# Kernel tuning notes

Measured on AMD Instinct MI355X. Metric: run time of the kernel, lower is better.

The kernel has to match this reference:

```python
import jax, jax.numpy as jnp
import numpy as np

D_MODEL = 1024
NUM_HEADS = 16
HEAD_DIM = D_MODEL // NUM_HEADS
THETA = 10000.0
BATCH, SEQ = 2, 2048


def rope(x, token_positions):
    # x: [b, h, s, d]; token_positions: [s]
    d = x.shape[-1]
    freqs = 1.0 / THETA ** (jnp.arange(0, d, 2, dtype=jnp.float32)[: d // 2] / d)
    ang = token_positions.astype(jnp.float32)[:, None] * freqs[None, :]  # [s, d/2]
    cos, sin = jnp.cos(ang), jnp.sin(ang)
    xr = x.reshape(*x.shape[:-1], d // 2, 2)
    x_even, x_odd = xr[..., 0], xr[..., 1]
    out_even = x_even * cos - x_odd * sin
    out_odd = x_even * sin + x_odd * cos
    return jnp.stack([out_even, out_odd], axis=-1).reshape(x.shape)


def setup_inputs() -> dict:
    key = jax.random.key(0)
    ks = jax.random.split(key, 5)
    std = np.sqrt(2.0 / (D_MODEL + D_MODEL))
    mk = lambda k: (jax.random.truncated_normal(k, -3.0, 3.0, (D_MODEL, D_MODEL), jnp.float32) * std)
    return {
        "x": jax.random.normal(ks[0], (BATCH, SEQ, D_MODEL), jnp.float32),
        "Wq": mk(ks[1]),
        "Wk": mk(ks[2]),
        "Wv": mk(ks[3]),
        "Wo": mk(ks[4]),
        "casual_mask": jnp.tril(jnp.ones((SEQ, SEQ), dtype=bool)),
        "token_positions": jnp.arange(SEQ, dtype=jnp.int32),
    }


def reference(x, Wq, Wk, Wv, Wo, casual_mask, token_positions):
    b, s, _ = x.shape
    split = lambda t: t.reshape(b, s, NUM_HEADS, HEAD_DIM).transpose(0, 2, 1, 3)
    q = split(x @ Wq.T)  # [b, h, s, d]
    k = split(x @ Wk.T)
    v = split(x @ Wv.T)
    q = rope(q, token_positions)
    k = rope(k, token_positions)
    scores = jnp.einsum("bhqd,bhkd->bhqk", q, k) / np.sqrt(HEAD_DIM)
    scores = jnp.where(casual_mask, scores, -jnp.inf)
    probs = jax.nn.softmax(scores, axis=-1)
    out = jnp.einsum("bhqk,bhkd->bhqd", probs, v)
    out = out.transpose(0, 2, 1, 3).reshape(b, s, D_MODEL)
    return out @ Wo.T
```

## Files before the change

### kernel.cpp

```cpp
#include <hip/hip_runtime.h>
#include <hip/hip_bf16.h>

#define SEQ_LEN 2048
#define NBATCH 2
#define DM 1024
#define NH 16
#define HD 64
#define NR (NBATCH * SEQ_LEN)
#define NQKV (3 * DM)
#define LDQK 2048

typedef __attribute__((ext_vector_type(8))) short bf16x8;
typedef __attribute__((ext_vector_type(4))) float f32x4;
typedef __attribute__((ext_vector_type(16))) float f32x16;

__device__ __forceinline__ short f2b(float f) {
    __hip_bfloat16 h = __float2bfloat16(f);
    return *reinterpret_cast<short*>(&h);
}

__device__ __forceinline__ void gload_lds16(const void* g, void* l) {
    __builtin_amdgcn_global_load_lds(
        (const __attribute__((address_space(1))) unsigned int*)g,
        (__attribute__((address_space(3))) unsigned int*)l, 16, 0, 0);
}

__global__ __launch_bounds__(256) void cvt_all(
    const float* __restrict__ x,  const float* __restrict__ wq,
    const float* __restrict__ wk, const float* __restrict__ wv,
    const float* __restrict__ wo,
    __hip_bfloat16* __restrict__ xb, __hip_bfloat16* __restrict__ wqkvb,
    __hip_bfloat16* __restrict__ wob) {
    int id = blockIdx.x;
    const float* src; __hip_bfloat16* dst;
    if (id < 4096) { src = x + (size_t)id * 1024; dst = xb + (size_t)id * 1024; }
    else {
        int k = id - 4096, seg = k >> 10;
        size_t off = (size_t)(k & 1023) * 1024;
        if      (seg == 0) { src = wq + off; dst = wqkvb + off; }
        else if (seg == 1) { src = wk + off; dst = wqkvb + (1u << 20) + off; }
        else if (seg == 2) { src = wv + off; dst = wqkvb + (2u << 20) + off; }
        else               { src = wo + off; dst = wob + off; }
    }
    int i = threadIdx.x * 4;
    float4 v = *(const float4*)(src + i);
    dst[i + 0] = __float2bfloat16(v.x);
    dst[i + 1] = __float2bfloat16(v.y);
    dst[i + 2] = __float2bfloat16(v.z);
    dst[i + 3] = __float2bfloat16(v.w);
}

__device__ __forceinline__ void store_c(float* p, float v) { *p = v; }
__device__ __forceinline__ void store_c(__hip_bfloat16* p, float v) {
    *p = __float2bfloat16(v);
}

template <typename CT, bool FUSED>
__global__ __launch_bounds__(256) void gemm128(
    const __hip_bfloat16* __restrict__ A,
    const __hip_bfloat16* __restrict__ B,
    CT* __restrict__ C, int K, int ldc,
    __hip_bfloat16* __restrict__ Vtg, const int* __restrict__ pos, int nbx) {
    __shared__ __hip_bfloat16 As[2][128 * 32];
    __shared__ __hip_bfloat16 Bs[2][128 * 32];
    const int t    = threadIdx.x;
    const int wave = t >> 6;
    const int lane = t & 63;
    const int quad = lane >> 4;
    const int l16  = lane & 15;
    const int wy = wave >> 1, wx = wave & 1;

    const int nwg = gridDim.x;
    const int wg  = (blockIdx.x & 7) * (nwg >> 3) + (blockIdx.x >> 3);
    const int bx  = wg % nbx;
    const int by  = wg / nbx;
    const int m0 = bx * 128, n0 = by * 128;

    const int sr  = t >> 2;
    const int scx = (t & 3) ^ (sr & 3);

    const __hip_bfloat16* Ag = A + (size_t)(m0 + sr) * K + scx * 8;
    const __hip_bfloat16* Bg = B + (size_t)(n0 + sr) * K + scx * 8;

#define GSTAGE(BUF, K0)                                                         \
    {                                                                           \
        gload_lds16(Ag + (K0), (char*)As[BUF] + t * 16);                        \
        gload_lds16(Ag + (size_t)64 * K + (K0), (char*)As[BUF] + (t + 256) * 16); \
        gload_lds16(Bg + (K0), (char*)Bs[BUF] + t * 16);                        \
        gload_lds16(Bg + (size_t)64 * K + (K0), (char*)Bs[BUF] + (t + 256) * 16); \
    }

    f32x4 acc[4][4];
#pragma unroll
    for (int i = 0; i < 4; i++)
#pragma unroll
        for (int j = 0; j < 4; j++) acc[i][j] = (f32x4){0.f, 0.f, 0.f, 0.f};

    const int NT = K >> 5;
    GSTAGE(0, 0);
    __syncthreads();
    int cur = 0;
    for (int t32 = 0; t32 < NT; ++t32) {
        if (t32 + 1 < NT) GSTAGE(cur ^ 1, (t32 + 1) * 32);

        bf16x8 af[4], bfr[4];
#pragma unroll
        for (int rb = 0; rb < 4; rb++) {
            int row = wy * 64 + rb * 16 + l16;
            af[rb] = *(const bf16x8*)((const char*)As[cur] + row * 64 +
                                      ((quad ^ (row & 3)) << 4));
        }
#pragma unroll
        for (int cb = 0; cb < 4; cb++) {
            int row = wx * 64 + cb * 16 + l16;
            bfr[cb] = *(const bf16x8*)((const char*)Bs[cur] + row * 64 +
                                       ((quad ^ (row & 3)) << 4));
        }
#pragma unroll
        for (int rb = 0; rb < 4; rb++)
#pragma unroll
            for (int cb = 0; cb < 4; cb++)
                acc[rb][cb] = __builtin_amdgcn_mfma_f32_16x16x32_bf16(
                    af[rb], bfr[cb], acc[rb][cb], 0, 0, 0);

        __syncthreads();
        cur ^= 1;
    }
#undef GSTAGE

    if (!FUSED || by < 16) {
        if constexpr (FUSED) {
            const float sc = (by < 8) ? 0.125f : 1.0f;
            float fr[4];
#pragma unroll
            for (int cb = 0; cb < 4; cb++) {
                int i = ((cb * 16 + l16) & 63) >> 1;
                fr[cb] = __expf(-(float)(2 * i) * (9.210340371976184f / 64.0f));
            }
            const float par = (l16 & 1) ? 1.f : -1.f;
#pragma unroll
            for (int rb = 0; rb < 4; rb++)
#pragma unroll
                for (int r = 0; r < 4; r++) {
                    int row = m0 + wy * 64 + rb * 16 + quad * 4 + r;
                    float p = (float)pos[row & (SEQ_LEN - 1)];
#pragma unroll
                    for (int cb = 0; cb < 4; cb++) {
                        float sn, cs;
                        __sincosf(p * fr[cb], &sn, &cs);
                        float v  = acc[rb][cb][r];
                        float pt = __shfl_xor(v, 1);
                        acc[rb][cb][r] = (v * cs + par * pt * sn) * sc;
                    }
                }
        }
#pragma unroll
        for (int rb = 0; rb < 4; rb++)
#pragma unroll
            for (int r = 0; r < 4; r++) {
                size_t ro = (size_t)(m0 + wy * 64 + rb * 16 + quad * 4 + r) * ldc;
#pragma unroll
                for (int cb = 0; cb < 4; cb++)
                    store_c(&C[ro + n0 + wx * 64 + cb * 16 + l16], acc[rb][cb][r]);
            }
    } else {
#pragma unroll
        for (int rb = 0; rb < 4; rb++) {
            int row0 = m0 + wy * 64 + rb * 16 + quad * 4;
            int bb = row0 >> 11, ss = row0 & (SEQ_LEN - 1);
            int ssw = (ss & ~12) | ((ss & 4) << 1) | ((ss & 8) >> 1);
#pragma unroll
            for (int cb = 0; cb < 4; cb++) {
                int vcol = n0 + wx * 64 + cb * 16 + l16 - 2048;
                int hh = vcol >> 6, dd = vcol & 63;
                ushort4 u;
                u.x = (unsigned short)f2b(acc[rb][cb][0]);
                u.y = (unsigned short)f2b(acc[rb][cb][1]);
                u.z = (unsigned short)f2b(acc[rb][cb][2]);
                u.w = (unsigned short)f2b(acc[rb][cb][3]);
                *(ushort4*)(Vtg + ((size_t)(bb * NH + hh) * HD + dd) * SEQ_LEN + ssw) = u;
            }
        }
    }
}

__global__ __launch_bounds__(256, 2) void attn_kernel(
    const __hip_bfloat16* __restrict__ QK,
    const __hip_bfloat16* __restrict__ Vtg,
    __hip_bfloat16* __restrict__ O) {
    __shared__ __hip_bfloat16 Ks[2][64 * 64];
    __shared__ __hip_bfloat16 Vs[2][64 * 64];

    const int t    = threadIdx.x;
    const int wave = t >> 6;
    const int lane = t & 63;
    const int l5   = lane & 31;
    const int hi   = lane >> 5;
    const int id   = blockIdx.x;
    const int qtc  = id >> 5;
    const int hb   = id & 31;
    const int h    = hb & 15;
    const int b    = hb >> 4;
    const int qt   = (qtc < 8) ? (15 - qtc) : (qtc - 8);

    const int row0 = qt * 128 + wave * 32;
    const int ktd  = (row0 + 31) >> 6;
    const int KTM  = 2 * qt + 1;

    const int sr  = t >> 3;
    const int scx = (t & 7) ^ (sr & 7);

    const __hip_bfloat16* kbase = QK + (size_t)(b * SEQ_LEN) * LDQK + DM + h * HD;
    const __hip_bfloat16* vbase = Vtg + (size_t)((b * NH + h) * HD) * SEQ_LEN;

    bf16x8 qf[4];
    {
        const __hip_bfloat16* qp =
            QK + (size_t)(b * SEQ_LEN + row0 + l5) * LDQK + h * HD + hi * 8;
#pragma unroll
        for (int dc = 0; dc < 4; dc++) qf[dc] = *(const bf16x8*)(qp + dc * 16);
    }

    f32x16 o0, o1;
#pragma unroll
    for (int i = 0; i < 16; i++) { o0[i] = 0.f; o1[i] = 0.f; }
    float l_acc = 0.f;

#define STAGE(BUF, KT)                                                          \
    {                                                                           \
        gload_lds16(kbase + (size_t)((KT) * 64 + sr) * LDQK + scx * 8,          \
                    (char*)&Ks[BUF][0] + t * 16);                               \
        gload_lds16(kbase + (size_t)((KT) * 64 + sr + 32) * LDQK + scx * 8,     \
                    (char*)&Ks[BUF][0] + (t + 256) * 16);                       \
        gload_lds16(vbase + (size_t)sr * SEQ_LEN + (KT) * 64 + scx * 8,         \
                    (char*)&Vs[BUF][0] + t * 16);                               \
        gload_lds16(vbase + (size_t)(sr + 32) * SEQ_LEN + (KT) * 64 + scx * 8,  \
                    (char*)&Vs[BUF][0] + (t + 256) * 16);                       \
    }

#define LFRAG(BASE, ROW, CH)                                                    \
    (*(const bf16x8*)((const char*)(BASE) + (ROW) * 128 + ((((CH) ^ ((ROW) & 7))) << 4)))

#define MKPA(S, PA0, PA1)                                                       \
    {                                                                           \
        float p_[16];                                                           \
        _Pragma("unroll") for (int r = 0; r < 16; r++) {                        \
            p_[r] = __expf((S)[r]);                                             \
            l_acc += p_[r];                                                     \
        }                                                                       \
        _Pragma("unroll") for (int j = 0; j < 8; j++) {                         \
            PA0[j] = f2b(p_[j]);                                                \
            PA1[j] = f2b(p_[8 + j]);                                            \
        }                                                                       \
    }

#define TRIP(BUF, KT)                                                           \
    {                                                                           \
        f32x16 s0, s1;                                                          \
        _Pragma("unroll") for (int i = 0; i < 16; i++) { s0[i] = 0.f; s1[i] = 0.f; } \
        __builtin_amdgcn_s_setprio(1);                                          \
        _Pragma("unroll") for (int dc = 0; dc < 4; dc++) {                      \
            bf16x8 k0f = LFRAG(Ks[BUF], l5, dc * 2 + hi);                       \
            bf16x8 k1f = LFRAG(Ks[BUF], 32 + l5, dc * 2 + hi);                  \
            s0 = __builtin_amdgcn_mfma_f32_32x32x16_bf16(k0f, qf[dc], s0, 0, 0, 0); \
            s1 = __builtin_amdgcn_mfma_f32_32x32x16_bf16(k1f, qf[dc], s1, 0, 0, 0); \
        }                                                                       \
        __builtin_amdgcn_s_setprio(0);                                          \
        if ((KT) == ktd) {                \
            int qrow = row0 + l5;                                               \
            _Pragma("unroll") for (int r = 0; r < 16; r++) {                    \
                int key = (KT) * 64 + (r & 3) + 8 * (r >> 2) + 4 * hi;          \
                if (key > qrow) s0[r] = -1e30f;                                 \
                if (key + 32 > qrow) s1[r] = -1e30f;                            \
            }                                                                   \
        }                                                                       \
        bf16x8 pa0, pa1, pa2, pa3;                                              \
        MKPA(s0, pa0, pa1);                                                     \
        MKPA(s1, pa2, pa3);                                                     \
        __builtin_amdgcn_s_setprio(1);                                          \
        _Pragma("unroll") for (int kc = 0; kc < 4; kc++) {                      \
            bf16x8 v0f = LFRAG(Vs[BUF], l5, kc * 2 + hi);                       \
            bf16x8 v1f = LFRAG(Vs[BUF], 32 + l5, kc * 2 + hi);                  \
            bf16x8 paf = (kc == 0) ? pa0 : (kc == 1) ? pa1 : (kc == 2) ? pa2 : pa3; \
            o0 = __builtin_amdgcn_mfma_f32_32x32x16_bf16(paf, v0f, o0, 0, 0, 0); \
            o1 = __builtin_amdgcn_mfma_f32_32x32x16_bf16(paf, v1f, o1, 0, 0, 0); \
        }                                                                       \
        __builtin_amdgcn_s_setprio(0);                                          \
    }

    STAGE(0, 0);
    for (int kt = 0; kt <= KTM; ++kt) {
        const int buf = kt & 1;
        __syncthreads();
        if (kt < KTM) STAGE(buf ^ 1, kt + 1);
        if (kt <= ktd) TRIP(buf, kt);
    }

    l_acc += __shfl_xor(l_acc, 32);
    float inv = 1.0f / l_acc;
#pragma unroll
    for (int r = 0; r < 16; r++) {
        int crow  = (r & 3) + 8 * (r >> 2) + 4 * hi;
        float invr = __shfl(inv, crow);
        size_t ro = (size_t)(b * SEQ_LEN + row0 + crow) * DM + h * HD;
        O[ro + l5]      = __float2bfloat16(o0[r] * invr);
        O[ro + 32 + l5] = __float2bfloat16(o1[r] * invr);
    }
#undef STAGE
#undef LFRAG
#undef MKPA
#undef TRIP
}

extern "C" void kernel_launch(void* const* d_in, const int* in_sizes, int n_in,
                              void* d_out, int out_size, void* d_ws, size_t ws_size,
                              hipStream_t stream) {
    const float* x  = (const float*)d_in[0];
    const float* Wq = (const float*)d_in[1];
    const float* Wk = (const float*)d_in[2];
    const float* Wv = (const float*)d_in[3];
    const float* Wo = (const float*)d_in[4];
    const int* pos = (const int*)d_in[6];
    float* out = (float*)d_out;

    char* w = (char*)d_ws;
    const size_t MiB = 1024 * 1024;
    __hip_bfloat16* xb    = (__hip_bfloat16*)(w + 0 * MiB);
    __hip_bfloat16* Ab    = (__hip_bfloat16*)(w + 0 * MiB);
    __hip_bfloat16* Wqkvb = (__hip_bfloat16*)(w + 8 * MiB);
    __hip_bfloat16* Wob   = (__hip_bfloat16*)(w + 14 * MiB);
    __hip_bfloat16* QKb   = (__hip_bfloat16*)(w + 16 * MiB);
    __hip_bfloat16* Vtg   = (__hip_bfloat16*)(w + 32 * MiB);

    cvt_all<<<8192, 256, 0, stream>>>(x, Wq, Wk, Wv, Wo, xb, Wqkvb, Wob);

    gemm128<__hip_bfloat16, true><<<(NR / 128) * (NQKV / 128), 256, 0, stream>>>(
        xb, Wqkvb, QKb, DM, LDQK, Vtg, pos, NR / 128);

    attn_kernel<<<512, 256, 0, stream>>>(QKb, Vtg, Ab);

    gemm128<float, false><<<(NR / 128) * (DM / 128), 256, 0, stream>>>(
        Ab, Wob, out, DM, DM, nullptr, nullptr, NR / 128);
}
```

Before: 196.5 us.

## Replace QKV projection GEMM with 256x256-tile, 8-wave pipelined kernel

Adds a dedicated QKV projection kernel that uses 256x256 output tiles with 512 threads, split into quarter-tile LDS stages that are double-buffered. Global loads are interleaved with the MFMA sub-blocks and controlled by explicit vmcnt waits and barriers. The RoPE, scaling and V-transpose epilogue are reimplemented inline. The larger tiles increase data reuse and cut global traffic per FLOP. In exchange the grid drops to 192 workgroups, which may underfill the 256 CUs, and register pressure goes up.

```diff
diff --git a/kernel.cpp b/kernel.cpp
--- a/kernel.cpp
+++ b/kernel.cpp
@@ -55,6 +55,197 @@
     *p = __float2bfloat16(v);
 }
 
+__global__ __launch_bounds__(512) void gemm256_qkv(
+    const __hip_bfloat16* __restrict__ A,
+    const __hip_bfloat16* __restrict__ B,
+    __hip_bfloat16* __restrict__ C,
+    __hip_bfloat16* __restrict__ Vtg,
+    const int* __restrict__ pos) {
+    __shared__ __hip_bfloat16 As[2][2][64 * 128];
+    __shared__ __hip_bfloat16 Bs[2][2][64 * 128];
+
+    const int t    = threadIdx.x;
+    const int wave = t >> 6;
+    const int wm   = wave >> 2;
+    const int wn   = wave & 3;
+    const int lane = t & 63;
+    const int quad = lane >> 4;
+    const int l16  = lane & 15;
+    const int K    = DM;
+    const int NT   = K >> 6;
+    const int NI   = K >> 7;
+
+    const int wg = (blockIdx.x & 7) * 24 + (blockIdx.x >> 3);
+    const int bx = wg & 15;
+    const int by = wg >> 4;
+    const int m0 = bx * 256, n0 = by * 256;
+
+    const int  t16  = t * 16;
+    const int  scx8 = ((t & 7) ^ ((t >> 3) & 7)) * 8;
+    const int  srA  = t >> 3;
+    const int  gB   = (t >> 8) & 1;
+    const int  rB   = (t >> 3) & 31;
+
+#define STAGE_A(BUF, HM, TT)                                                    \
+    {                                                                           \
+        const __hip_bfloat16* _s =                                              \
+            A + (size_t)(m0 + (HM) * 64 + srA) * K + (TT) * 64 + scx8;          \
+        gload_lds16(_s,               (char*)As[BUF][HM] + t16);                \
+        gload_lds16(_s + (size_t)128 * K, (char*)As[BUF][HM] + t16 + 8192);     \
+    }
+#define STAGE_B(BUF, HN, TT)                                                    \
+    {                                                                           \
+        const __hip_bfloat16* _s =                                              \
+            B + (size_t)(n0 + gB * 64 + (HN) * 32 + rB) * K + (TT) * 64 + scx8; \
+        gload_lds16(_s,               (char*)Bs[BUF][HN] + t16);                \
+        gload_lds16(_s + (size_t)128 * K, (char*)Bs[BUF][HN] + t16 + 8192);     \
+    }
+#define LDA(BUF, HM, AF)                                                        \
+    _Pragma("unroll") for (int rb = 0; rb < 4; rb++)                            \
+    _Pragma("unroll") for (int kk = 0; kk < 2; kk++)                            \
+        AF[rb][kk] = *(const bf16x8*)((const char*)As[BUF][HM] +                \
+            (wm * 64 + rb * 16 + l16) * 128 + (((kk * 4 + quad) ^ (l16 & 7)) << 4));
+#define LDB(BUF, HN, BF)                                                        \
+    _Pragma("unroll") for (int cb = 0; cb < 2; cb++)                            \
+    _Pragma("unroll") for (int kk = 0; kk < 2; kk++)                            \
+        BF[cb][kk] = *(const bf16x8*)((const char*)Bs[BUF][HN] +                \
+            (wn * 32 + cb * 16 + l16) * 128 + (((kk * 4 + quad) ^ (l16 & 7)) << 4));
+#define MM(HM, HN, AF, BF)                                                      \
+    {                                                                           \
+        __builtin_amdgcn_s_setprio(1);                                          \
+        _Pragma("unroll") for (int rb = 0; rb < 4; rb++)                        \
+        _Pragma("unroll") for (int cb = 0; cb < 2; cb++) {                      \
+            acc[HM][HN][rb][cb] = __builtin_amdgcn_mfma_f32_16x16x32_bf16(      \
+                AF[rb][0], BF[cb][0], acc[HM][HN][rb][cb], 0, 0, 0);            \
+            acc[HM][HN][rb][cb] = __builtin_amdgcn_mfma_f32_16x16x32_bf16(      \
+                AF[rb][1], BF[cb][1], acc[HM][HN][rb][cb], 0, 0, 0);            \
+        }                                                                       \
+        __builtin_amdgcn_s_setprio(0);                                          \
+    }
+#define VM0 asm volatile("s_waitcnt vmcnt(0)" ::: "memory")
+#define VM4 asm volatile("s_waitcnt vmcnt(4)" ::: "memory")
+#define VM6 asm volatile("s_waitcnt vmcnt(6)" ::: "memory")
+#define BARR __builtin_amdgcn_s_barrier()
+
+    f32x4 acc[2][2][4][2];
+#pragma unroll
+    for (int a_ = 0; a_ < 2; a_++)
+#pragma unroll
+        for (int b_ = 0; b_ < 2; b_++)
+#pragma unroll
+            for (int c_ = 0; c_ < 4; c_++)
+#pragma unroll
+                for (int d_ = 0; d_ < 2; d_++)
+                    acc[a_][b_][c_][d_] = (f32x4){0.f, 0.f, 0.f, 0.f};
+
+    STAGE_A(0, 0, 0); STAGE_A(0, 1, 0); STAGE_B(0, 0, 0); STAGE_B(0, 1, 0);
+    STAGE_A(1, 0, 1); STAGE_B(1, 0, 1); STAGE_A(1, 1, 1);
+    VM6;
+    BARR;
+
+    for (int i = 0; i < NI; ++i) {
+        const int TB = 2 * i + 1, T2 = 2 * i + 2, T3 = 2 * i + 3;
+        const bool s2 = T2 < NT, s3 = T3 < NT;
+        bf16x8 a[4][2], b0[2][2], b1[2][2];
+
+        LDA(0, 0, a); LDB(0, 0, b0);
+        STAGE_B(1, 1, TB);
+        MM(0, 0, a, b0);
+        BARR;
+        LDB(0, 1, b1);
+        if (s2) STAGE_A(0, 0, T2);
+        MM(0, 1, a, b1);
+        BARR;
+        LDA(0, 1, a); LDB(0, 0, b0);
+        MM(1, 0, a, b0);
+        BARR;
+        LDB(0, 1, b1);
+        if (s2) STAGE_B(0, 0, T2);
+        MM(1, 1, a, b1);
+        if (i < NI - 1) { VM4; } else { VM0; }
+        BARR;
+        LDA(1, 0, a); LDB(1, 0, b0);
+        if (s2) STAGE_A(0, 1, T2);
+        MM(0, 0, a, b0);
+        BARR;
+        LDB(1, 1, b1);
+        if (s2) STAGE_B(0, 1, T2);
+        if (s3) STAGE_A(1, 0, T3);
+        MM(0, 1, a, b1);
+        BARR;
+        LDA(1, 1, a); LDB(1, 0, b0);
+        MM(1, 0, a, b0);
+        BARR;
+        LDB(1, 1, b1);
+        if (s3) { STAGE_B(1, 0, T3); STAGE_A(1, 1, T3); }
+        MM(1, 1, a, b1);
+        if (i < NI - 1) { VM6; BARR; }
+    }
+#undef STAGE_A
+#undef STAGE_B
+#undef LDA
+#undef LDB
+#undef MM
+#undef VM0
+#undef VM4
+#undef VM6
+#undef BARR
+
+    if (by < 8) {
+        const float sc = (by < 4) ? 0.125f : 1.0f;
+        float fr[2][2];
+#pragma unroll
+        for (int hn = 0; hn < 2; hn++)
+#pragma unroll
+            for (int cb = 0; cb < 2; cb++)
+                fr[hn][cb] = __expf(-(float)((hn * 32 + cb * 16 + l16) & ~1) *
+                                    (9.210340371976184f / 64.0f));
+        const float par = (l16 & 1) ? 1.f : -1.f;
+#pragma unroll
+        for (int hm = 0; hm < 2; hm++)
+#pragma unroll
+            for (int rb = 0; rb < 4; rb++)
+#pragma unroll
+                for (int r = 0; r < 4; r++) {
+                    int row = m0 + wm * 128 + hm * 64 + rb * 16 + quad * 4 + r;
+                    float p = (float)pos[row & (SEQ_LEN - 1)];
+#pragma unroll
+                    for (int hn = 0; hn < 2; hn++)
+#pragma unroll
+                        for (int cb = 0; cb < 2; cb++) {
+                            float sn, cs;
+                            __sincosf(p * fr[hn][cb], &sn, &cs);
+                            float v  = acc[hm][hn][rb][cb][r];
+                            float pt = __shfl_xor(v, 1);
+                            C[(size_t)row * LDQK + n0 + wn * 64 + hn * 32 + cb * 16 + l16] =
+                                __float2bfloat16((v * cs + par * pt * sn) * sc);
+                        }
+                }
+    } else {
+#pragma unroll
+        for (int hm = 0; hm < 2; hm++)
+#pragma unroll
+            for (int rb = 0; rb < 4; rb++) {
+                int row0e = m0 + wm * 128 + hm * 64 + rb * 16 + quad * 4;
+                int bb = row0e >> 11, ss = row0e & (SEQ_LEN - 1);
+                int ssw = (ss & ~12) | ((ss & 4) << 1) | ((ss & 8) >> 1);
+#pragma unroll
+                for (int hn = 0; hn < 2; hn++)
+#pragma unroll
+                    for (int cb = 0; cb < 2; cb++) {
+                        int vcol = n0 + wn * 64 + hn * 32 + cb * 16 + l16 - 2048;
+                        int hh = vcol >> 6, dd = vcol & 63;
+                        ushort4 u;
+                        u.x = (unsigned short)f2b(acc[hm][hn][rb][cb][0]);
+                        u.y = (unsigned short)f2b(acc[hm][hn][rb][cb][1]);
+                        u.z = (unsigned short)f2b(acc[hm][hn][rb][cb][2]);
+                        u.w = (unsigned short)f2b(acc[hm][hn][rb][cb][3]);
+                        *(ushort4*)(Vtg + ((size_t)(bb * NH + hh) * HD + dd) * SEQ_LEN + ssw) = u;
+                    }
+            }
+    }
+}
+
 template <typename CT, bool FUSED>
 __global__ __launch_bounds__(256) void gemm128(
     const __hip_bfloat16* __restrict__ A,
@@ -266,7 +457,7 @@
             s1 = __builtin_amdgcn_mfma_f32_32x32x16_bf16(k1f, qf[dc], s1, 0, 0, 0); \
         }                                                                       \
         __builtin_amdgcn_s_setprio(0);                                          \
-        if ((KT) == ktd) {                \
+        if ((KT) == ktd) {                                                      \
             int qrow = row0 + l5;                                               \
             _Pragma("unroll") for (int r = 0; r < 16; r++) {                    \
                 int key = (KT) * 64 + (r & 3) + 8 * (r >> 2) + 4 * hi;          \
@@ -334,8 +525,7 @@
 
     cvt_all<<<8192, 256, 0, stream>>>(x, Wq, Wk, Wv, Wo, xb, Wqkvb, Wob);
 
-    gemm128<__hip_bfloat16, true><<<(NR / 128) * (NQKV / 128), 256, 0, stream>>>(
-        xb, Wqkvb, QKb, DM, LDQK, Vtg, pos, NR / 128);
+    gemm256_qkv<<<192, 512, 0, stream>>>(xb, Wqkvb, QKb, Vtg, pos);
 
     attn_kernel<<<512, 256, 0, stream>>>(QKb, Vtg, Ab);
 
```

Result: no change. 198.2 us (+0.8%).
